# Optimization experiments

Measured on AMD Instinct MI355X. Metric: run time of the kernel, lower is better.

The kernel has to match this reference:

```python
import jax, jax.numpy as jnp
import numpy as np

DIM = 512; H = 56; W = 56; HEADS = 16; WS = 7; SHIFT = 3; MLP_RATIO = 4.0; B = 16
N = WS * WS              # tokens per window = 49
NW = (H // WS) * (W // WS)  # 64 windows
HID = int(DIM * MLP_RATIO)


def _rel_pos_index():
    coords = np.stack(np.meshgrid(np.arange(WS), np.arange(WS), indexing='ij')).reshape(2, -1)
    rel = (coords[:, :, None] - coords[:, None, :]).transpose(1, 2, 0)
    rel[..., 0] += WS - 1
    rel[..., 1] += WS - 1
    rel[..., 0] *= 2 * WS - 1
    return rel.sum(-1).astype(np.int32)  # (N, N)


def _attn_mask():
    # standard SW-MSA mask: 0 within same region, -100 across regions
    img = np.zeros((H, W), np.float32)
    cnt = 0
    sl = (slice(0, -WS), slice(-WS, -SHIFT), slice(-SHIFT, None))
    for hs in sl:
        for ws_ in sl:
            img[hs, ws_] = cnt
            cnt += 1
    mw = img.reshape(H // WS, WS, W // WS, WS).transpose(0, 2, 1, 3).reshape(-1, N)  # (NW, N)
    am = mw[:, None, :] - mw[:, :, None]
    return np.where(am != 0, np.float32(-100.0), np.float32(0.0))  # (NW, N, N)


def setup_inputs() -> dict:
    key = jax.random.key(0)
    ks = jax.random.split(key, 6)
    s = jnp.float32(0.02)
    return {
        'x': jax.random.normal(ks[0], (B, H * W, DIM), jnp.float32),
        'qkv_w': jax.random.normal(ks[1], (3 * DIM, DIM), jnp.float32) * s,  # layout (h dh 3) x C
        'qkv_b': jnp.zeros((3 * DIM,), jnp.float32),
        'out_w': jax.random.normal(ks[2], (DIM, DIM), jnp.float32) * s,
        'out_b': jnp.zeros((DIM,), jnp.float32),
        'rp_bias_table': jax.random.normal(ks[3], ((2 * WS - 1) ** 2, HEADS), jnp.float32) * s,
        'fc1_w': jax.random.normal(ks[4], (HID, DIM), jnp.float32) * s,
        'fc1_b': jnp.zeros((HID,), jnp.float32),
        'fc2_w': jax.random.normal(ks[5], (DIM, HID), jnp.float32) * s,
        'fc2_b': jnp.zeros((DIM,), jnp.float32),
        'ln1_w': jnp.ones((DIM,), jnp.float32),
        'ln1_b': jnp.zeros((DIM,), jnp.float32),
        'ln2_w': jnp.ones((DIM,), jnp.float32),
        'ln2_b': jnp.zeros((DIM,), jnp.float32),
        'attn_mask': jnp.asarray(_attn_mask()),
        'rp_index': jnp.asarray(_rel_pos_index()),
    }


def _ln(x, w, b):
    m = x.mean(-1, keepdims=True)
    v = ((x - m) ** 2).mean(-1, keepdims=True)
    return (x - m) * jax.lax.rsqrt(v + 1e-5) * w + b


def reference(x, qkv_w, qkv_b, out_w, out_b, rp_bias_table, fc1_w, fc1_b, fc2_w, fc2_b,
              ln1_w, ln1_b, ln2_w, ln2_b, attn_mask, rp_index):
    Bx, L, C = x.shape
    dh = C // HEADS
    scale = jnp.float32(dh) ** -0.5

    shortcut = x
    y = _ln(x, ln1_w, ln1_b).reshape(Bx, H, W, C)
    y = jnp.roll(y, (-SHIFT, -SHIFT), axis=(1, 2))
    # window partition -> (B*NW, N, C)
    xw = y.reshape(Bx, H // WS, WS, W // WS, WS, C).transpose(0, 1, 3, 2, 4, 5).reshape(-1, N, C)

    qkv = (xw @ qkv_w.T + qkv_b).reshape(-1, N, HEADS, dh, 3).transpose(4, 0, 2, 1, 3)
    q, k, v = qkv[0] * scale, qkv[1], qkv[2]          # (B_, h, N, dh)
    attn = jnp.einsum('bhnd,bhmd->bhnm', q, k)        # (B_, h, N, N)

    bias = rp_bias_table[rp_index.reshape(-1)].reshape(N, N, HEADS).transpose(2, 0, 1)
    attn = attn + 2.0 * bias                          # source adds the bias twice (faithful)
    attn = attn.reshape(Bx, NW, HEADS, N, N) + attn_mask[None, :, None]
    attn = jax.nn.softmax(attn, axis=-1).reshape(-1, HEADS, N, N)

    o = jnp.einsum('bhnm,bhmd->bhnd', attn, v).transpose(0, 2, 1, 3).reshape(-1, N, C)
    o = o @ out_w.T + out_b
    # window reverse + roll back
    o = o.reshape(Bx, H // WS, W // WS, WS, WS, C).transpose(0, 1, 3, 2, 4, 5).reshape(Bx, H, W, C)
    o = jnp.roll(o, (SHIFT, SHIFT), axis=(1, 2)).reshape(Bx, L, C)

    x = shortcut + o
    h2 = _ln(x, ln2_w, ln2_b)
    h2 = jax.nn.gelu(h2 @ fc1_w.T + fc1_b, approximate=False) @ fc2_w.T + fc2_b
    return x + h2
```

## Files before the change

kernel.cpp:

```cpp
#include <hip/hip_runtime.h>
#include <hip/hip_bf16.h>

#define CDIM 512
#define NHEADS 16
#define DH 32
#define NTOK 49
#define NWIN 64
#define BATCH 16
#define HH 56
#define WW 56
#define LTOK 3136
#define TTOK 50176
#define HID 2048
#define SHIFT_ 3

typedef short bf16x8 __attribute__((ext_vector_type(8)));
typedef float f32x4 __attribute__((ext_vector_type(4)));

__device__ __forceinline__ float b2f(unsigned int u) {
    return __uint_as_float((u & 0xffffu) << 16);
}
__device__ __forceinline__ unsigned short f2b(float f) {
    __hip_bfloat16 h = __float2bfloat16(f);
    return *reinterpret_cast<unsigned short*>(&h);
}
__device__ __forceinline__ void load8(const unsigned short* p, float* f) {
    uint4 r = *reinterpret_cast<const uint4*>(p);
    f[0] = b2f(r.x); f[1] = b2f(r.x >> 16);
    f[2] = b2f(r.y); f[3] = b2f(r.y >> 16);
    f[4] = b2f(r.z); f[5] = b2f(r.z >> 16);
    f[6] = b2f(r.w); f[7] = b2f(r.w >> 16);
}
__device__ __forceinline__ uint4 pack8(const float* f) {
    uint4 r;
    r.x = (unsigned)f2b(f[0]) | ((unsigned)f2b(f[1]) << 16);
    r.y = (unsigned)f2b(f[2]) | ((unsigned)f2b(f[3]) << 16);
    r.z = (unsigned)f2b(f[4]) | ((unsigned)f2b(f[5]) << 16);
    r.w = (unsigned)f2b(f[6]) | ((unsigned)f2b(f[7]) << 16);
    return r;
}
__device__ __forceinline__ bool probe_f32(const unsigned* p) { return p[0] == 0x3F800000u; }
__device__ __forceinline__ float ld1(const void* p, size_t i, bool f32) {
    return f32 ? ((const float*)p)[i] : b2f(((const unsigned short*)p)[i]);
}
__device__ __forceinline__ void load8_any(const void* p, size_t idx, bool f32, float* f) {
    if (f32) {
        const float4* q = (const float4*)((const float*)p + idx);
        float4 a = q[0], b = q[1];
        f[0]=a.x; f[1]=a.y; f[2]=a.z; f[3]=a.w; f[4]=b.x; f[5]=b.y; f[6]=b.z; f[7]=b.w;
    } else {
        load8((const unsigned short*)p + idx, f);
    }
}

#define GLOAD_LDS16(g, l) \
    __builtin_amdgcn_global_load_lds( \
        (const __attribute__((address_space(1))) unsigned int*)(g), \
        (__attribute__((address_space(3))) unsigned int*)(l), 16, 0, 0)

__global__ __launch_bounds__(256)
void cvt_kernel(const void* __restrict__ in, unsigned short* __restrict__ out,
                const unsigned* __restrict__ probe)
{
    bool f32in = probe_f32(probe);
    size_t idx = ((size_t)blockIdx.x * 256 + threadIdx.x) * 8;
    float f[8];
    load8_any(in, idx, f32in, f);
    *reinterpret_cast<uint4*>(out + idx) = pack8(f);
}

__global__ __launch_bounds__(256)
void cmb_kernel(const void* __restrict__ rp_tab, const int* __restrict__ rp_idx,
                const void* __restrict__ mask, unsigned short* __restrict__ cmb,
                const unsigned* __restrict__ probe)
{
    bool f32in = probe_f32(probe);
    int wh = blockIdx.x;
    int wi = wh >> 4, h = wh & 15;
    for (int e = threadIdx.x; e < 4096; e += 256) {
        int q = e >> 6, k = e & 63;
        float v = -1e30f;
        if (q < NTOK && k < NTOK) {
            int bi = rp_idx[q * NTOK + k];
            v = 2.0f * ld1(rp_tab, (size_t)bi * NHEADS + h, f32in)
              + ld1(mask, (size_t)wi * NTOK * NTOK + (size_t)q * NTOK + k, f32in);
        }
        cmb[(size_t)wh * 4096 + e] = f2b(v);
    }
}

template<int SHIFTED, int XRAW>
__global__ __launch_bounds__(256)
void ln_kernel(const void* __restrict__ xin,
               const void* __restrict__ gw,
               const void* __restrict__ gb,
               unsigned short* __restrict__ out,
               const unsigned* __restrict__ probe)
{
    bool f32in = probe_f32(probe);
    int wid = threadIdx.x >> 6, lane = threadIdx.x & 63;
    int tok = blockIdx.x * 4 + wid;
    int c0 = lane * 8;
    float xs[8];
    load8_any(xin, (size_t)tok * CDIM + c0, XRAW && f32in, xs);
    float s = 0.f, s2 = 0.f;
#pragma unroll
    for (int j = 0; j < 8; ++j) { s += xs[j]; s2 += xs[j] * xs[j]; }
#pragma unroll
    for (int off = 32; off; off >>= 1) { s += __shfl_xor(s, off); s2 += __shfl_xor(s2, off); }
    float mean = s * (1.0f / CDIM);
    float var = s2 * (1.0f / CDIM) - mean * mean;
    float rstd = rsqrtf(var + 1e-5f);
    float wv[8], bv[8], ov[8];
    load8_any(gw, c0, f32in, wv);
    load8_any(gb, c0, f32in, bv);
#pragma unroll
    for (int j = 0; j < 8; ++j) ov[j] = (xs[j] - mean) * rstd * wv[j] + bv[j];
    size_t dst;
    if (SHIFTED) {
        int b = tok / LTOK, l = tok % LTOK;
        int h = l / WW, w = l % WW;
        int hs = (h + HH - SHIFT_) % HH;
        int ws_ = (w + WW - SHIFT_) % WW;
        int wh = hs / 7, ii = hs % 7, wwi = ws_ / 7, jj = ws_ % 7;
        int t = (b * NWIN + wh * 8 + wwi) * NTOK + ii * 7 + jj;
        dst = (size_t)t * CDIM + c0;
    } else {
        dst = (size_t)tok * CDIM + c0;
    }
    *reinterpret_cast<uint4*>(out + dst) = pack8(ov);
}

template<int EPI>
__global__ __launch_bounds__(256)
void gemm_kernel(const unsigned short* __restrict__ A,
                 const unsigned short* __restrict__ Wbf,
                 const void* __restrict__ bias,
                 const void* __restrict__ aux,
                 void* __restrict__ out0,
                 unsigned short* __restrict__ out1,
                 unsigned short* __restrict__ out2,
                 int K, int moff,
                 const unsigned* __restrict__ probe)
{
    bool f32in = probe_f32(probe);
    __shared__ __align__(16) unsigned short sA[128 * 32];
    __shared__ __align__(16) unsigned short sB[128 * 32];
    int tid = threadIdx.x;
    int wave = tid >> 6, lane = tid & 63, quad = lane >> 4, l16 = lane & 15;
    int bm = blockIdx.x, bn = blockIdx.y;
    int wm = (wave & 1) * 64, wn = (wave >> 1) * 64;

    const unsigned short* aP = A   + (size_t)(bm * 128 + (tid >> 2)) * K + (tid & 3) * 8;
    const unsigned short* bP = Wbf + (size_t)(bn * 128 + (tid >> 2)) * K + (tid & 3) * 8;
    const size_t rowhop = (size_t)64 * K;
    char* lA = (char*)sA + tid * 16;
    char* lB = (char*)sB + tid * 16;

    f32x4 acc[16];
#pragma unroll
    for (int t = 0; t < 16; ++t) acc[t] = (f32x4){0.f, 0.f, 0.f, 0.f};

    for (int k0 = 0; k0 < K; k0 += 32) {
        __syncthreads();
        GLOAD_LDS16(aP + k0,          lA);
        GLOAD_LDS16(aP + k0 + rowhop, lA + 4096);
        GLOAD_LDS16(bP + k0,          lB);
        GLOAD_LDS16(bP + k0 + rowhop, lB + 4096);
        __syncthreads();
        bf16x8 af[4], bfr[4];
#pragma unroll
        for (int am = 0; am < 4; ++am)
            af[am] = *reinterpret_cast<const bf16x8*>(&sA[(wm + am * 16 + l16) * 32 + quad * 8]);
#pragma unroll
        for (int bn_ = 0; bn_ < 4; ++bn_)
            bfr[bn_] = *reinterpret_cast<const bf16x8*>(&sB[(wn + bn_ * 16 + l16) * 32 + quad * 8]);
#pragma unroll
        for (int am = 0; am < 4; ++am)
#pragma unroll
            for (int bn_ = 0; bn_ < 4; ++bn_)
                acc[am * 4 + bn_] = __builtin_amdgcn_mfma_f32_16x16x32_bf16(
                    af[am], bfr[bn_], acc[am * 4 + bn_], 0, 0, 0);
    }

#pragma unroll
    for (int am = 0; am < 4; ++am) {
#pragma unroll
        for (int bn_ = 0; bn_ < 4; ++bn_) {
#pragma unroll
            for (int r = 0; r < 4; ++r) {
                int gm = bm * 128 + wm + am * 16 + quad * 4 + r;
                int gn = bn * 128 + wn + bn_ * 16 + l16;
                float v = acc[am * 4 + bn_][r] + ld1(bias, gn, f32in);
                if (EPI == 0) {
                    int s = gn % 3, q = gn / 3;
                    int d = q & 31, h = q >> 5;
                    int w = gm / NTOK, n = gm % NTOK;
                    size_t dst = ((size_t)(w * NHEADS + h) * NTOK + n) * DH + d;
                    if (s == 0)      ((unsigned short*)out0)[dst] = f2b(v * 0.17677669529663687f);
                    else if (s == 1) out1[dst] = f2b(v);
                    else             out2[dst] = f2b(v);
                } else if (EPI == 1) {
                    int w = gm / NTOK, n = gm % NTOK;
                    int b = w >> 6, wi = w & 63;
                    int wh = wi >> 3, wwi = wi & 7;
                    int ii = n / 7, jj = n % 7;
                    int h_ = (wh * 7 + ii + SHIFT_) % HH;
                    int w_ = (wwi * 7 + jj + SHIFT_) % WW;
                    size_t dst = ((size_t)b * LTOK + h_ * WW + w_) * CDIM + gn;
                    v += ld1(aux, dst, f32in);
                    ((unsigned short*)out0)[dst] = f2b(v);
                } else if (EPI == 2) {
                    float g = 0.5f * v * (1.0f + erff(v * 0.70710678118654752f));
                    ((unsigned short*)out0)[(size_t)gm * HID + gn] = f2b(g);
                } else {
                    size_t dst = (size_t)(moff + gm) * CDIM + gn;
                    v += b2f(((const unsigned short*)aux)[dst]);
                    if (f32in) ((float*)out0)[dst] = v;
                    else       ((unsigned short*)out0)[dst] = f2b(v);
                }
            }
        }
    }
}

__global__ __launch_bounds__(256)
void attn_kernel(const unsigned short* __restrict__ Qb,
                 const unsigned short* __restrict__ Kb,
                 const unsigned short* __restrict__ Vb,
                 const unsigned short* __restrict__ cmb,
                 unsigned short* __restrict__ Ob)
{
    __shared__ __align__(16) unsigned short Pl[4][64 * 72];
    int wid = threadIdx.x >> 6, lane = threadIdx.x & 63;
    int l16 = lane & 15, quad = lane >> 4;
    int wi = blockIdx.x >> 6, rem = blockIdx.x & 63;
    int b = rem >> 2, hq = rem & 3;
    int h = hq * 4 + wid;
    int bw = b * NWIN + wi;
    size_t base = (size_t)(bw * NHEADS + h) * (NTOK * DH);
    const unsigned short* cmbp = cmb + (size_t)(wi * NHEADS + h) * 4096;

    bf16x8 kf[4], qf[4];
#pragma unroll
    for (int t = 0; t < 4; ++t) {
        kf[t] = *reinterpret_cast<const bf16x8*>(Kb + base + (t * 16 + l16) * DH + quad * 8);
        qf[t] = *reinterpret_cast<const bf16x8*>(Qb + base + (t * 16 + l16) * DH + quad * 8);
    }
    f32x4 s[4][4];
#pragma unroll
    for (int kt = 0; kt < 4; ++kt)
#pragma unroll
        for (int nt = 0; nt < 4; ++nt)
            s[kt][nt] = (f32x4){0.f, 0.f, 0.f, 0.f};
#pragma unroll
    for (int kt = 0; kt < 4; ++kt)
#pragma unroll
        for (int nt = 0; nt < 4; ++nt)
            s[kt][nt] = __builtin_amdgcn_mfma_f32_16x16x32_bf16(kf[kt], qf[nt], s[kt][nt], 0, 0, 0);

    float mx[4] = {-1e30f, -1e30f, -1e30f, -1e30f}, sm[4] = {0.f, 0.f, 0.f, 0.f};
#pragma unroll
    for (int kt = 0; kt < 4; ++kt)
#pragma unroll
        for (int nt = 0; nt < 4; ++nt) {
            uint2 cv = *reinterpret_cast<const uint2*>(cmbp + (nt * 16 + l16) * 64 + kt * 16 + quad * 4);
            float c[4] = {b2f(cv.x), b2f(cv.x >> 16), b2f(cv.y), b2f(cv.y >> 16)};
#pragma unroll
            for (int r = 0; r < 4; ++r) {
                float sv = s[kt][nt][r] + c[r];
                s[kt][nt][r] = sv;
                mx[nt] = fmaxf(mx[nt], sv);
            }
        }
#pragma unroll
    for (int nt = 0; nt < 4; ++nt) {
        mx[nt] = fmaxf(mx[nt], __shfl_xor(mx[nt], 16));
        mx[nt] = fmaxf(mx[nt], __shfl_xor(mx[nt], 32));
    }
#pragma unroll
    for (int kt = 0; kt < 4; ++kt)
#pragma unroll
        for (int nt = 0; nt < 4; ++nt)
#pragma unroll
            for (int r = 0; r < 4; ++r) {
                float pv = expf(s[kt][nt][r] - mx[nt]);
                s[kt][nt][r] = pv;
                sm[nt] += pv;
            }
    float rs[4];
#pragma unroll
    for (int nt = 0; nt < 4; ++nt) {
        sm[nt] += __shfl_xor(sm[nt], 16);
        sm[nt] += __shfl_xor(sm[nt], 32);
        rs[nt] = 1.0f / sm[nt];
    }
    unsigned short* P = Pl[wid];
#pragma unroll
    for (int kt = 0; kt < 4; ++kt)
#pragma unroll
        for (int nt = 0; nt < 4; ++nt) {
            uint2 w;
            w.x = (unsigned)f2b(s[kt][nt][0] * rs[nt]) | ((unsigned)f2b(s[kt][nt][1] * rs[nt]) << 16);
            w.y = (unsigned)f2b(s[kt][nt][2] * rs[nt]) | ((unsigned)f2b(s[kt][nt][3] * rs[nt]) << 16);
            *reinterpret_cast<uint2*>(&P[(nt * 16 + l16) * 72 + kt * 16 + quad * 4]) = w;
        }

    f32x4 o[4][2];
#pragma unroll
    for (int mt = 0; mt < 4; ++mt)
#pragma unroll
        for (int n2 = 0; n2 < 2; ++n2)
            o[mt][n2] = (f32x4){0.f, 0.f, 0.f, 0.f};
#pragma unroll
    for (int ks = 0; ks < 2; ++ks) {
        bf16x8 pf[4];
#pragma unroll
        for (int mt = 0; mt < 4; ++mt)
            pf[mt] = *reinterpret_cast<const bf16x8*>(&P[(mt * 16 + l16) * 72 + ks * 32 + quad * 8]);
        bf16x8 vf[2];
#pragma unroll
        for (int n2 = 0; n2 < 2; ++n2) {
            union { bf16x8 v; unsigned short u[8]; } t;
#pragma unroll
            for (int j = 0; j < 8; ++j)
                t.u[j] = Vb[base + (size_t)(ks * 32 + quad * 8 + j) * DH + n2 * 16 + l16];
            vf[n2] = t.v;
        }
#pragma unroll
        for (int mt = 0; mt < 4; ++mt)
#pragma unroll
            for (int n2 = 0; n2 < 2; ++n2)
                o[mt][n2] = __builtin_amdgcn_mfma_f32_16x16x32_bf16(pf[mt], vf[n2], o[mt][n2], 0, 0, 0);
    }
#pragma unroll
    for (int mt = 0; mt < 4; ++mt)
#pragma unroll
        for (int n2 = 0; n2 < 2; ++n2)
#pragma unroll
            for (int r = 0; r < 4; ++r) {
                int q = mt * 16 + quad * 4 + r;
                if (q < NTOK)
                    Ob[((size_t)bw * NTOK + q) * CDIM + h * DH + n2 * 16 + l16] = f2b(o[mt][n2][r]);
            }
}

extern "C" void kernel_launch(void* const* d_in, const int* in_sizes, int n_in,
                              void* d_out, int out_size, void* d_ws, size_t ws_size,
                              hipStream_t stream)
{
    const void* x      = d_in[0];
    const void* qkv_w  = d_in[1];
    const void* qkv_b  = d_in[2];
    const void* out_w  = d_in[3];
    const void* out_b  = d_in[4];
    const void* rp_tab = d_in[5];
    const void* fc1_w  = d_in[6];
    const void* fc1_b  = d_in[7];
    const void* fc2_w  = d_in[8];
    const void* fc2_b  = d_in[9];
    const void* ln1_w  = d_in[10];
    const void* ln1_b  = d_in[11];
    const void* ln2_w  = d_in[12];
    const void* ln2_b  = d_in[13];
    const void* amask  = d_in[14];
    const int*  rp_idx = (const int*)d_in[15];
    const unsigned* probe = (const unsigned*)ln1_w;

    unsigned short* ws = (unsigned short*)d_ws;
    const size_t SZ = (size_t)TTOK * CDIM;
    unsigned short* xw = ws;
    unsigned short* Qb = ws + SZ;
    unsigned short* Kb = ws + 2 * SZ;
    unsigned short* Vb = ws + 3 * SZ;
    unsigned short* Ob = ws + 4 * SZ;
    unsigned short* Cmb = ws;
    unsigned short* X1 = ws;
    unsigned short* Hb = ws + SZ;
    unsigned short* fc1wbf = ws + 3 * SZ;
    unsigned short* fc2wbf = ws + 3 * SZ + (size_t)HID * CDIM;
    unsigned short* L2 = ws + 4 * SZ;
    unsigned short* qkvwbf = (unsigned short*)d_out;
    unsigned short* outwbf = qkvwbf + (size_t)3 * CDIM * CDIM;
    if (ws_size < 5 * SZ * sizeof(unsigned short)) return;

    const int HM = TTOK / 2;

    cvt_kernel<<<(3 * CDIM * CDIM) / 2048, 256, 0, stream>>>(qkv_w, qkvwbf, probe);
    cvt_kernel<<<(CDIM * CDIM) / 2048, 256, 0, stream>>>(out_w, outwbf, probe);

    ln_kernel<1, 1><<<TTOK / 4, 256, 0, stream>>>(x, ln1_w, ln1_b, xw, probe);
    gemm_kernel<0><<<dim3(TTOK / 128, (3 * CDIM) / 128), 256, 0, stream>>>(
        xw, qkvwbf, qkv_b, nullptr, Qb, Kb, Vb, CDIM, 0, probe);
    cmb_kernel<<<1024, 256, 0, stream>>>(rp_tab, rp_idx, amask, Cmb, probe);
    attn_kernel<<<4096, 256, 0, stream>>>(Qb, Kb, Vb, Cmb, Ob);

    cvt_kernel<<<(HID * CDIM) / 2048, 256, 0, stream>>>(fc1_w, fc1wbf, probe);
    cvt_kernel<<<(HID * CDIM) / 2048, 256, 0, stream>>>(fc2_w, fc2wbf, probe);

    gemm_kernel<1><<<dim3(TTOK / 128, CDIM / 128), 256, 0, stream>>>(
        Ob, outwbf, out_b, x, X1, nullptr, nullptr, CDIM, 0, probe);
    ln_kernel<0, 0><<<TTOK / 4, 256, 0, stream>>>(X1, ln2_w, ln2_b, L2, probe);

    for (int half = 0; half < 2; ++half) {
        size_t mo = (size_t)half * HM;
        gemm_kernel<2><<<dim3(HM / 128, HID / 128), 256, 0, stream>>>(
            L2 + mo * CDIM, fc1wbf, fc1_b, nullptr, Hb, nullptr, nullptr, CDIM, 0, probe);
        gemm_kernel<3><<<dim3(HM / 128, CDIM / 128), 256, 0, stream>>>(
            Hb, fc2wbf, fc2_b, X1, d_out, nullptr, nullptr, HID, (int)mo, probe);
    }
}
```

Measured before the change: 1.228 ms.

## Double-buffer GEMM LDS tiles, swap grid order, permute QKV weights for cheaper epilogue

The GEMM kernel now uses two LDS buffers and prefetches the next K tile with global_load_lds while MFMAs run on the current one, which drops one barrier per iteration. The grid is transposed so consecutive blocks share the same A row-tile, improving L2 reuse of activations. QKV weight rows are permuted at conversion time so the epilogue picks the q/k/v destination and scale once per column instead of using div/mod per element. LDS use doubles, which may lower occupancy.

```diff
diff --git a/kernel.cpp b/kernel.cpp
--- a/kernel.cpp
+++ b/kernel.cpp
@@ -70,6 +70,20 @@
 }
 
 __global__ __launch_bounds__(256)
+void cvt_qkvw_kernel(const void* __restrict__ in, unsigned short* __restrict__ out,
+                     const unsigned* __restrict__ probe)
+{
+    bool f32in = probe_f32(probe);
+    int r = blockIdx.x * 4 + (threadIdx.x >> 6);
+    int lane = threadIdx.x & 63;
+    int s = r >> 9, q = r & 511, h = q >> 5, d = q & 31;
+    int orow = h * 96 + d * 3 + s;
+    float f[8];
+    load8_any(in, (size_t)orow * CDIM + lane * 8, f32in, f);
+    *reinterpret_cast<uint4*>(out + (size_t)r * CDIM + lane * 8) = pack8(f);
+}
+
+__global__ __launch_bounds__(256)
 void cmb_kernel(const void* __restrict__ rp_tab, const int* __restrict__ rp_idx,
                 const void* __restrict__ mask, unsigned short* __restrict__ cmb,
                 const unsigned* __restrict__ probe)
@@ -144,80 +158,104 @@
                  const unsigned* __restrict__ probe)
 {
     bool f32in = probe_f32(probe);
-    __shared__ __align__(16) unsigned short sA[128 * 32];
-    __shared__ __align__(16) unsigned short sB[128 * 32];
+    __shared__ __align__(16) unsigned short sA[2][128 * 32];
+    __shared__ __align__(16) unsigned short sB[2][128 * 32];
     int tid = threadIdx.x;
     int wave = tid >> 6, lane = tid & 63, quad = lane >> 4, l16 = lane & 15;
-    int bm = blockIdx.x, bn = blockIdx.y;
+    int bn = blockIdx.x, bm = blockIdx.y;
     int wm = (wave & 1) * 64, wn = (wave >> 1) * 64;
 
     const unsigned short* aP = A   + (size_t)(bm * 128 + (tid >> 2)) * K + (tid & 3) * 8;
     const unsigned short* bP = Wbf + (size_t)(bn * 128 + (tid >> 2)) * K + (tid & 3) * 8;
     const size_t rowhop = (size_t)64 * K;
-    char* lA = (char*)sA + tid * 16;
-    char* lB = (char*)sB + tid * 16;
+    const int loff = tid * 16;
 
     f32x4 acc[16];
 #pragma unroll
     for (int t = 0; t < 16; ++t) acc[t] = (f32x4){0.f, 0.f, 0.f, 0.f};
 
-    for (int k0 = 0; k0 < K; k0 += 32) {
-        __syncthreads();
-        GLOAD_LDS16(aP + k0,          lA);
-        GLOAD_LDS16(aP + k0 + rowhop, lA + 4096);
-        GLOAD_LDS16(bP + k0,          lB);
-        GLOAD_LDS16(bP + k0 + rowhop, lB + 4096);
-        __syncthreads();
+    GLOAD_LDS16(aP,          (char*)sA[0] + loff);
+    GLOAD_LDS16(aP + rowhop, (char*)sA[0] + loff + 4096);
+    GLOAD_LDS16(bP,          (char*)sB[0] + loff);
+    GLOAD_LDS16(bP + rowhop, (char*)sB[0] + loff + 4096);
+    __syncthreads();
+
+    const int NT = K >> 5;
+    int cur = 0;
+    for (int t = 0; t < NT; ++t) {
+        if (t + 1 < NT) {
+            int k0 = (t + 1) << 5;
+            char* dA = (char*)sA[cur ^ 1] + loff;
+            char* dB = (char*)sB[cur ^ 1] + loff;
+            GLOAD_LDS16(aP + k0,          dA);
+            GLOAD_LDS16(aP + k0 + rowhop, dA + 4096);
+            GLOAD_LDS16(bP + k0,          dB);
+            GLOAD_LDS16(bP + k0 + rowhop, dB + 4096);
+        }
+        const unsigned short* cA = sA[cur];
+        const unsigned short* cB = sB[cur];
         bf16x8 af[4], bfr[4];
 #pragma unroll
         for (int am = 0; am < 4; ++am)
-            af[am] = *reinterpret_cast<const bf16x8*>(&sA[(wm + am * 16 + l16) * 32 + quad * 8]);
+            af[am] = *reinterpret_cast<const bf16x8*>(&cA[(wm + am * 16 + l16) * 32 + quad * 8]);
 #pragma unroll
         for (int bn_ = 0; bn_ < 4; ++bn_)
-            bfr[bn_] = *reinterpret_cast<const bf16x8*>(&sB[(wn + bn_ * 16 + l16) * 32 + quad * 8]);
+            bfr[bn_] = *reinterpret_cast<const bf16x8*>(&cB[(wn + bn_ * 16 + l16) * 32 + quad * 8]);
 #pragma unroll
         for (int am = 0; am < 4; ++am)
 #pragma unroll
             for (int bn_ = 0; bn_ < 4; ++bn_)
                 acc[am * 4 + bn_] = __builtin_amdgcn_mfma_f32_16x16x32_bf16(
                     af[am], bfr[bn_], acc[am * 4 + bn_], 0, 0, 0);
-    }
-
-#pragma unroll
-    for (int am = 0; am < 4; ++am) {
-#pragma unroll
-        for (int bn_ = 0; bn_ < 4; ++bn_) {
-#pragma unroll
-            for (int r = 0; r < 4; ++r) {
-                int gm = bm * 128 + wm + am * 16 + quad * 4 + r;
-                int gn = bn * 128 + wn + bn_ * 16 + l16;
-                float v = acc[am * 4 + bn_][r] + ld1(bias, gn, f32in);
-                if (EPI == 0) {
-                    int s = gn % 3, q = gn / 3;
-                    int d = q & 31, h = q >> 5;
-                    int w = gm / NTOK, n = gm % NTOK;
+        __syncthreads();
+        cur ^= 1;
+    }
+
+#pragma unroll
+    for (int bn_ = 0; bn_ < 4; ++bn_) {
+        int gn = bn * 128 + wn + bn_ * 16 + l16;
+        if (EPI == 0) {
+            int s = gn >> 9, h = (gn >> 5) & 15, d = gn & 31;
+            float bv = ld1(bias, h * 96 + d * 3 + s, f32in);
+            unsigned short* outp = (s == 0) ? (unsigned short*)out0 : (s == 1 ? out1 : out2);
+            float mul = (s == 0) ? 0.17677669529663687f : 1.0f;
+#pragma unroll
+            for (int am = 0; am < 4; ++am) {
+#pragma unroll
+                for (int r = 0; r < 4; ++r) {
+                    int gm = bm * 128 + wm + am * 16 + quad * 4 + r;
+                    int w = gm / NTOK, n = gm - w * NTOK;
                     size_t dst = ((size_t)(w * NHEADS + h) * NTOK + n) * DH + d;
-                    if (s == 0)      ((unsigned short*)out0)[dst] = f2b(v * 0.17677669529663687f);
-                    else if (s == 1) out1[dst] = f2b(v);
-                    else             out2[dst] = f2b(v);
-                } else if (EPI == 1) {
-                    int w = gm / NTOK, n = gm % NTOK;
-                    int b = w >> 6, wi = w & 63;
-                    int wh = wi >> 3, wwi = wi & 7;
-                    int ii = n / 7, jj = n % 7;
-                    int h_ = (wh * 7 + ii + SHIFT_) % HH;
-                    int w_ = (wwi * 7 + jj + SHIFT_) % WW;
-                    size_t dst = ((size_t)b * LTOK + h_ * WW + w_) * CDIM + gn;
-                    v += ld1(aux, dst, f32in);
-                    ((unsigned short*)out0)[dst] = f2b(v);
-                } else if (EPI == 2) {
-                    float g = 0.5f * v * (1.0f + erff(v * 0.70710678118654752f));
-                    ((unsigned short*)out0)[(size_t)gm * HID + gn] = f2b(g);
-                } else {
-                    size_t dst = (size_t)(moff + gm) * CDIM + gn;
-                    v += b2f(((const unsigned short*)aux)[dst]);
-                    if (f32in) ((float*)out0)[dst] = v;
-                    else       ((unsigned short*)out0)[dst] = f2b(v);
+                    outp[dst] = f2b((acc[am * 4 + bn_][r] + bv) * mul);
+                }
+            }
+        } else {
+            float bv = ld1(bias, gn, f32in);
+#pragma unroll
+            for (int am = 0; am < 4; ++am) {
+#pragma unroll
+                for (int r = 0; r < 4; ++r) {
+                    int gm = bm * 128 + wm + am * 16 + quad * 4 + r;
+                    float v = acc[am * 4 + bn_][r] + bv;
+                    if (EPI == 1) {
+                        int w = gm / NTOK, n = gm - w * NTOK;
+                        int b = w >> 6, wi = w & 63;
+                        int wh = wi >> 3, wwi = wi & 7;
+                        int ii = n / 7, jj = n - ii * 7;
+                        int h_ = (wh * 7 + ii + SHIFT_) % HH;
+                        int w_ = (wwi * 7 + jj + SHIFT_) % WW;
+                        size_t dst = ((size_t)b * LTOK + h_ * WW + w_) * CDIM + gn;
+                        v += ld1(aux, dst, f32in);
+                        ((unsigned short*)out0)[dst] = f2b(v);
+                    } else if (EPI == 2) {
+                        float g = 0.5f * v * (1.0f + erff(v * 0.70710678118654752f));
+                        ((unsigned short*)out0)[(size_t)gm * HID + gn] = f2b(g);
+                    } else {
+                        size_t dst = (size_t)(moff + gm) * CDIM + gn;
+                        v += b2f(((const unsigned short*)aux)[dst]);
+                        if (f32in) ((float*)out0)[dst] = v;
+                        else       ((unsigned short*)out0)[dst] = f2b(v);
+                    }
                 }
             }
         }
@@ -386,11 +424,11 @@
 
     const int HM = TTOK / 2;
 
-    cvt_kernel<<<(3 * CDIM * CDIM) / 2048, 256, 0, stream>>>(qkv_w, qkvwbf, probe);
+    cvt_qkvw_kernel<<<(3 * CDIM) / 4, 256, 0, stream>>>(qkv_w, qkvwbf, probe);
     cvt_kernel<<<(CDIM * CDIM) / 2048, 256, 0, stream>>>(out_w, outwbf, probe);
 
     ln_kernel<1, 1><<<TTOK / 4, 256, 0, stream>>>(x, ln1_w, ln1_b, xw, probe);
-    gemm_kernel<0><<<dim3(TTOK / 128, (3 * CDIM) / 128), 256, 0, stream>>>(
+    gemm_kernel<0><<<dim3((3 * CDIM) / 128, TTOK / 128), 256, 0, stream>>>(
         xw, qkvwbf, qkv_b, nullptr, Qb, Kb, Vb, CDIM, 0, probe);
     cmb_kernel<<<1024, 256, 0, stream>>>(rp_tab, rp_idx, amask, Cmb, probe);
     attn_kernel<<<4096, 256, 0, stream>>>(Qb, Kb, Vb, Cmb, Ob);
@@ -398,15 +436,15 @@
     cvt_kernel<<<(HID * CDIM) / 2048, 256, 0, stream>>>(fc1_w, fc1wbf, probe);
     cvt_kernel<<<(HID * CDIM) / 2048, 256, 0, stream>>>(fc2_w, fc2wbf, probe);
 
-    gemm_kernel<1><<<dim3(TTOK / 128, CDIM / 128), 256, 0, stream>>>(
+    gemm_kernel<1><<<dim3(CDIM / 128, TTOK / 128), 256, 0, stream>>>(
         Ob, outwbf, out_b, x, X1, nullptr, nullptr, CDIM, 0, probe);
     ln_kernel<0, 0><<<TTOK / 4, 256, 0, stream>>>(X1, ln2_w, ln2_b, L2, probe);
 
     for (int half = 0; half < 2; ++half) {
         size_t mo = (size_t)half * HM;
-        gemm_kernel<2><<<dim3(HM / 128, HID / 128), 256, 0, stream>>>(
+        gemm_kernel<2><<<dim3(HID / 128, HM / 128), 256, 0, stream>>>(
             L2 + mo * CDIM, fc1wbf, fc1_b, nullptr, Hb, nullptr, nullptr, CDIM, 0, probe);
-        gemm_kernel<3><<<dim3(HM / 128, CDIM / 128), 256, 0, stream>>>(
+        gemm_kernel<3><<<dim3(CDIM / 128, HM / 128), 256, 0, stream>>>(
             Hb, fc2wbf, fc2_b, X1, d_out, nullptr, nullptr, HID, (int)mo, probe);
     }
 }
```

Result: faster. 1.151 ms (-6.3%).
